# Kernel optimization log

Hardware: AMD Instinct MI355X
Metric: run time of the kernel (lower is better)

The kernel has to match this reference:

```python
import jax, jax.numpy as jnp
import numpy as np

BS, SEQ_LEN, DIM = 8, 16, 512
DIM_QK, DIM_V = 512, 512
MAX_BS, MAX_SEQ = 8, 8192
START_POS = 4096
KV_LEN = START_POS + SEQ_LEN


def setup_inputs() -> dict:
    key = jax.random.key(0)
    ks = jax.random.split(key, 8)
    w_scale = 0.02
    return {
        "x": jax.random.normal(ks[0], (BS, SEQ_LEN, DIM), dtype=jnp.float32),
        "start_pos": START_POS,
        "mask": jnp.zeros((SEQ_LEN, KV_LEN), dtype=jnp.float32),
        "Wq": jax.random.normal(ks[1], (DIM_QK, DIM), dtype=jnp.float32) * w_scale,
        "Wk": jax.random.normal(ks[2], (DIM_QK, DIM), dtype=jnp.float32) * w_scale,
        "Wv": jax.random.normal(ks[3], (DIM_V, DIM), dtype=jnp.float32) * w_scale,
        "Wo": jax.random.normal(ks[4], (DIM, DIM_V), dtype=jnp.float32) * w_scale,
        "cache_k": jax.random.normal(ks[5], (MAX_BS, MAX_SEQ, DIM_QK), dtype=jnp.float32) * 0.1,
        "cache_v": jax.random.normal(ks[6], (MAX_BS, MAX_SEQ, DIM_V), dtype=jnp.float32) * 0.1,
    }


def reference(x, start_pos, mask, Wq, Wk, Wv, Wo, cache_k, cache_v):
    bs, seq_len, _ = x.shape
    dim_qk = Wq.shape[0]
    scale = (dim_qk // 2) ** (-0.5)  # note: source uses dim_qk//2, not dim_qk

    # projections (torch Linear: y = x @ W.T, W is [out, in])
    q = jnp.einsum('bsd,ed->bse', x, Wq)
    k = jnp.einsum('bsd,ed->bse', x, Wk)
    v = jnp.einsum('bsd,ed->bse', x, Wv)

    # KV-cache append + read (start_pos is static)
    cache_k = jax.lax.dynamic_update_slice(cache_k, k, (0, start_pos, 0))
    cache_v = jax.lax.dynamic_update_slice(cache_v, v, (0, start_pos, 0))
    k_full = cache_k[:bs, :start_pos + seq_len]  # [bs, kv_len, dim_qk]
    v_full = cache_v[:bs, :start_pos + seq_len]  # [bs, kv_len, dim_v]

    dist = jnp.einsum('bqd,bkd->bqk', q, k_full) * scale  # [bs, q, kv]
    weight = jax.lax.stop_gradient(dist)
    dist = dist + mask  # additive mask, broadcast over batch
    probs = jax.nn.softmax(dist, axis=-1)
    atten = jnp.einsum('bqk,bkv->bqv', probs, v_full)
    out = jnp.einsum('bqv,ev->bqe', atten, Wo)
    return (out, weight)
```

## Files before the change

### kernel.cpp

```cpp
#include <hip/hip_runtime.h>

#define BSZ 8
#define SEQ 16
#define DIMN 512
#define SP 4096
#define KVL 4112

#define SCALE 0.0625f

#define QBUF  0
#define KNEW  65536
#define VNEW  131072
#define PROBS 196608
#define APART 722944
#define ATTEN 4982784

__device__ __forceinline__ float tree16(const float* acc, bool b1, bool b2, bool b4, bool b8)
{
  float r8[8];
#pragma unroll
  for (int u = 0; u < 8; ++u) {
    float keep = b1 ? acc[u + 8] : acc[u];
    float send = b1 ? acc[u] : acc[u + 8];
    r8[u] = keep + __shfl_xor(send, 1);
  }
  float r4[4];
#pragma unroll
  for (int u = 0; u < 4; ++u) {
    float keep = b2 ? r8[u + 4] : r8[u];
    float send = b2 ? r8[u] : r8[u + 4];
    r4[u] = keep + __shfl_xor(send, 2);
  }
  float r2[2];
#pragma unroll
  for (int u = 0; u < 2; ++u) {
    float keep = b4 ? r4[u + 2] : r4[u];
    float send = b4 ? r4[u] : r4[u + 2];
    r2[u] = keep + __shfl_xor(send, 4);
  }
  float keep = b8 ? r2[1] : r2[0];
  float send = b8 ? r2[0] : r2[1];
  float r1 = keep + __shfl_xor(send, 8);
  r1 += __shfl_xor(r1, 16);
  r1 += __shfl_xor(r1, 32);
  return r1;
}

__global__ __launch_bounds__(256) void proj_dot(
    const float* __restrict__ X,
    const float* __restrict__ W0, const float* __restrict__ W1,
    const float* __restrict__ W2,
    float* __restrict__ D0, float* __restrict__ D1, float* __restrict__ D2)
{
  int b = blockIdx.x;
  int e0 = blockIdx.y * 32;
  int t = threadIdx.x, lane = t & 63, w = t >> 6;

  float4 xa[SEQ], xb[SEQ];
  const float* xbase = X + (size_t)b * SEQ * DIMN + lane * 8;
#pragma unroll
  for (int s = 0; s < SEQ; ++s) {
    xa[s] = *(const float4*)(xbase + s * DIMN);
    xb[s] = *(const float4*)(xbase + s * DIMN + 4);
  }

  bool b1 = (lane & 1), b2 = (lane & 2), b4 = (lane & 4), b8 = (lane & 8);
#pragma unroll 2
  for (int i = 0; i < 8; ++i) {
    int e = e0 + w + 4 * i;
    int m = e >> 9, col = e & 511;
    const float* W = (m == 0) ? W0 : (m == 1) ? W1 : W2;
    const float* wrow = W + (size_t)col * DIMN + lane * 8;
    float4 ka = *(const float4*)(wrow);
    float4 kb = *(const float4*)(wrow + 4);

    float acc[SEQ];
#pragma unroll
    for (int s = 0; s < SEQ; ++s) {
      acc[s] = xa[s].x * ka.x + xa[s].y * ka.y + xa[s].z * ka.z + xa[s].w * ka.w
             + xb[s].x * kb.x + xb[s].y * kb.y + xb[s].z * kb.z + xb[s].w * kb.w;
    }
    float r1 = tree16(acc, b1, b2, b4, b8);
    if (lane < 16) {
      int s = ((lane & 1) << 3) | ((lane & 2) << 1) | ((lane & 4) >> 1) | ((lane & 8) >> 3);
      float* D = (m == 0) ? D0 : (m == 1) ? D1 : D2;
      D[(size_t)(b * SEQ + s) * DIMN + col] = r1;
    }
  }
}

__global__ __launch_bounds__(256) void scores_kernel(
    const float* __restrict__ qbuf, const float* __restrict__ cache_k,
    const float* __restrict__ knew, float* __restrict__ weight)
{
  int b = blockIdx.x;
  int p0 = blockIdx.y * 64;
  int len = KVL - p0; if (len > 64) len = 64;
  int t = threadIdx.x, lane = t & 63, w = t >> 6;

  float4 qa[SEQ], qb[SEQ];
  const float* qbase = qbuf + (size_t)b * SEQ * DIMN + lane * 8;
#pragma unroll
  for (int s = 0; s < SEQ; ++s) {
    qa[s] = *(const float4*)(qbase + s * DIMN);
    qb[s] = *(const float4*)(qbase + s * DIMN + 4);
  }

  bool b1 = (lane & 1), b2 = (lane & 2), b4 = (lane & 4), b8 = (lane & 8);
  int niter = (len - w + 3) >> 2;
#pragma unroll 2
  for (int i = 0; i < niter; ++i) {
    int p = p0 + w + 4 * i;
    const float* krow = (p < SP)
        ? (cache_k + ((size_t)b * 8192 + p) * DIMN)
        : (knew + (size_t)(b * SEQ + (p - SP)) * DIMN);
    float4 ka = *(const float4*)(krow + lane * 8);
    float4 kb = *(const float4*)(krow + lane * 8 + 4);

    float acc[SEQ];
#pragma unroll
    for (int s = 0; s < SEQ; ++s) {
      acc[s] = qa[s].x * ka.x + qa[s].y * ka.y + qa[s].z * ka.z + qa[s].w * ka.w
             + qb[s].x * kb.x + qb[s].y * kb.y + qb[s].z * kb.z + qb[s].w * kb.w;
    }
    float r1 = tree16(acc, b1, b2, b4, b8);
    if (lane < 16) {
      int s = ((lane & 1) << 3) | ((lane & 2) << 1) | ((lane & 4) >> 1) | ((lane & 8) >> 3);
      weight[(size_t)(b * SEQ + s) * KVL + p] = r1 * SCALE;
    }
  }
}

__global__ __launch_bounds__(256) void softmax_kernel(
    const float* __restrict__ weight, const float* __restrict__ mask,
    float* __restrict__ probs)
{
  int row = blockIdx.x;
  int s = row & 15;
  int t = threadIdx.x, lane = t & 63, w = t >> 6;
  const float* src = weight + (size_t)row * KVL;
  const float* msk = mask + (size_t)s * KVL;

  float vals[17];
  float mx = -1e30f;
#pragma unroll
  for (int i = 0; i < 17; ++i) {
    int p = t + i * 256;
    if (p < KVL) { vals[i] = src[p] + msk[p]; mx = fmaxf(mx, vals[i]); }
    else vals[i] = -1e30f;
  }
  for (int off = 32; off >= 1; off >>= 1) mx = fmaxf(mx, __shfl_xor(mx, off));
  __shared__ float redm[4], reds[4];
  if (lane == 0) redm[w] = mx;
  __syncthreads();
  mx = fmaxf(fmaxf(redm[0], redm[1]), fmaxf(redm[2], redm[3]));

  float sum = 0.f;
#pragma unroll
  for (int i = 0; i < 17; ++i) {
    int p = t + i * 256;
    if (p < KVL) { vals[i] = __expf(vals[i] - mx); sum += vals[i]; }
  }
  for (int off = 32; off >= 1; off >>= 1) sum += __shfl_xor(sum, off);
  if (lane == 0) reds[w] = sum;
  __syncthreads();
  sum = reds[0] + reds[1] + reds[2] + reds[3];
  float inv = 1.0f / sum;

  float* dst = probs + (size_t)row * KVL;
#pragma unroll
  for (int i = 0; i < 17; ++i) {
    int p = t + i * 256;
    if (p < KVL) dst[p] = vals[i] * inv;
  }
}

__global__ __launch_bounds__(256) void attnv_kernel(
    const float* __restrict__ probs, const float* __restrict__ cache_v,
    const float* __restrict__ vnew, float* __restrict__ apart)
{
  __shared__ float pl[SEQ][64];
  int b = blockIdx.x, c = blockIdx.y;
  int p0 = c * 64;
  int len = KVL - p0; if (len > 64) len = 64;
  int t = threadIdx.x;

  for (int i = t; i < SEQ * 64; i += 256) {
    int q = i >> 6, j = i & 63;
    pl[q][j] = (j < len) ? probs[(size_t)(b * SEQ + q) * KVL + p0 + j] : 0.f;
  }
  __syncthreads();

  float acc0[SEQ], acc1[SEQ];
#pragma unroll
  for (int q = 0; q < SEQ; ++q) { acc0[q] = 0.f; acc1[q] = 0.f; }

  int nj4 = len >> 2;
  for (int j4 = 0; j4 < nj4; ++j4) {
    float4 pv[SEQ];
#pragma unroll
    for (int q = 0; q < SEQ; ++q) pv[q] = *(const float4*)&pl[q][j4 * 4];
#pragma unroll
    for (int jj = 0; jj < 4; ++jj) {
      int p = p0 + j4 * 4 + jj;
      const float* vrow = (p < SP)
          ? (cache_v + ((size_t)b * 8192 + p) * DIMN)
          : (vnew + (size_t)(b * SEQ + (p - SP)) * DIMN);
      float va = vrow[t], vb = vrow[t + 256];
#pragma unroll
      for (int q = 0; q < SEQ; ++q) {
        float pj = (jj == 0) ? pv[q].x : (jj == 1) ? pv[q].y : (jj == 2) ? pv[q].z : pv[q].w;
        acc0[q] += pj * va;
        acc1[q] += pj * vb;
      }
    }
  }
  float* outp = apart + (size_t)c * 65536 + (size_t)b * SEQ * DIMN;
#pragma unroll
  for (int q = 0; q < SEQ; ++q) {
    outp[q * DIMN + t] = acc0[q];
    outp[q * DIMN + t + 256] = acc1[q];
  }
}

__global__ __launch_bounds__(256) void reduce_att(
    const float* __restrict__ apart, float* __restrict__ atten)
{
  int idx = blockIdx.x * 256 + threadIdx.x;
  float s = 0.f;
  for (int c = 0; c < 65; ++c) s += apart[(size_t)c * 65536 + idx];
  atten[idx] = s;
}

extern "C" void kernel_launch(void* const* d_in, const int* in_sizes, int n_in,
                              void* d_out, int out_size, void* d_ws, size_t ws_size,
                              hipStream_t stream) {
  const float* x       = (const float*)d_in[0];
  const float* mask    = (const float*)d_in[2];
  const float* Wq      = (const float*)d_in[3];
  const float* Wk      = (const float*)d_in[4];
  const float* Wv      = (const float*)d_in[5];
  const float* Wo      = (const float*)d_in[6];
  const float* cache_k = (const float*)d_in[7];
  const float* cache_v = (const float*)d_in[8];
  float* out    = (float*)d_out;
  float* weight = out + 65536;
  float* ws     = (float*)d_ws;

  proj_dot<<<dim3(8, 48), 256, 0, stream>>>(
      x, Wq, Wk, Wv, ws + QBUF, ws + KNEW, ws + VNEW);
  scores_kernel<<<dim3(8, 65), 256, 0, stream>>>(ws + QBUF, cache_k, ws + KNEW, weight);
  softmax_kernel<<<dim3(128), 256, 0, stream>>>(weight, mask, ws + PROBS);
  attnv_kernel<<<dim3(8, 65), 256, 0, stream>>>(ws + PROBS, cache_v, ws + VNEW, ws + APART);
  reduce_att<<<dim3(256), 256, 0, stream>>>(ws + APART, ws + ATTEN);
  proj_dot<<<dim3(8, 16), 256, 0, stream>>>(
      ws + ATTEN, Wo, Wo, Wo, out, out, out);
}
```

Baseline: 310.0 us.

## Fuse scores, softmax and attn-V into a flash-decoding split-KV kernel

Merges the score, softmax and probability-times-V kernels into one kernel per (batch, 64-key chunk). Each block keeps its scores in shared memory, computes a local max and sum, and writes unnormalized partial outputs. A new reduce kernel rescales and combines the partials across chunks using the saved max and sum values. This drops the round-trip of the probability matrix through global memory and two kernel launches, at the cost of extra exp work and a heavier final reduction.

```diff
diff --git a/kernel.cpp b/kernel.cpp
--- a/kernel.cpp
+++ b/kernel.cpp
@@ -11,9 +11,11 @@
 #define QBUF  0
 #define KNEW  65536
 #define VNEW  131072
-#define PROBS 196608
-#define APART 722944
-#define ATTEN 4982784
+#define MLBUF 196608
+#define APART 213248
+#define ATTEN 4473088
+
+#define MLSTRIDE 8320
 
 __device__ __forceinline__ float tree16(const float* acc, bool b1, bool b2, bool b4, bool b8)
 {
@@ -89,105 +91,79 @@
   }
 }
 
-__global__ __launch_bounds__(256) void scores_kernel(
+__global__ __launch_bounds__(256) void fused_attn(
     const float* __restrict__ qbuf, const float* __restrict__ cache_k,
-    const float* __restrict__ knew, float* __restrict__ weight)
-{
-  int b = blockIdx.x;
-  int p0 = blockIdx.y * 64;
-  int len = KVL - p0; if (len > 64) len = 64;
-  int t = threadIdx.x, lane = t & 63, w = t >> 6;
-
-  float4 qa[SEQ], qb[SEQ];
-  const float* qbase = qbuf + (size_t)b * SEQ * DIMN + lane * 8;
-#pragma unroll
-  for (int s = 0; s < SEQ; ++s) {
-    qa[s] = *(const float4*)(qbase + s * DIMN);
-    qb[s] = *(const float4*)(qbase + s * DIMN + 4);
-  }
-
-  bool b1 = (lane & 1), b2 = (lane & 2), b4 = (lane & 4), b8 = (lane & 8);
-  int niter = (len - w + 3) >> 2;
-#pragma unroll 2
-  for (int i = 0; i < niter; ++i) {
-    int p = p0 + w + 4 * i;
-    const float* krow = (p < SP)
-        ? (cache_k + ((size_t)b * 8192 + p) * DIMN)
-        : (knew + (size_t)(b * SEQ + (p - SP)) * DIMN);
-    float4 ka = *(const float4*)(krow + lane * 8);
-    float4 kb = *(const float4*)(krow + lane * 8 + 4);
-
-    float acc[SEQ];
-#pragma unroll
-    for (int s = 0; s < SEQ; ++s) {
-      acc[s] = qa[s].x * ka.x + qa[s].y * ka.y + qa[s].z * ka.z + qa[s].w * ka.w
-             + qb[s].x * kb.x + qb[s].y * kb.y + qb[s].z * kb.z + qb[s].w * kb.w;
-    }
-    float r1 = tree16(acc, b1, b2, b4, b8);
-    if (lane < 16) {
-      int s = ((lane & 1) << 3) | ((lane & 2) << 1) | ((lane & 4) >> 1) | ((lane & 8) >> 3);
-      weight[(size_t)(b * SEQ + s) * KVL + p] = r1 * SCALE;
-    }
-  }
-}
-
-__global__ __launch_bounds__(256) void softmax_kernel(
-    const float* __restrict__ weight, const float* __restrict__ mask,
-    float* __restrict__ probs)
-{
-  int row = blockIdx.x;
-  int s = row & 15;
-  int t = threadIdx.x, lane = t & 63, w = t >> 6;
-  const float* src = weight + (size_t)row * KVL;
-  const float* msk = mask + (size_t)s * KVL;
-
-  float vals[17];
-  float mx = -1e30f;
-#pragma unroll
-  for (int i = 0; i < 17; ++i) {
-    int p = t + i * 256;
-    if (p < KVL) { vals[i] = src[p] + msk[p]; mx = fmaxf(mx, vals[i]); }
-    else vals[i] = -1e30f;
-  }
-  for (int off = 32; off >= 1; off >>= 1) mx = fmaxf(mx, __shfl_xor(mx, off));
-  __shared__ float redm[4], reds[4];
-  if (lane == 0) redm[w] = mx;
-  __syncthreads();
-  mx = fmaxf(fmaxf(redm[0], redm[1]), fmaxf(redm[2], redm[3]));
-
-  float sum = 0.f;
-#pragma unroll
-  for (int i = 0; i < 17; ++i) {
-    int p = t + i * 256;
-    if (p < KVL) { vals[i] = __expf(vals[i] - mx); sum += vals[i]; }
-  }
-  for (int off = 32; off >= 1; off >>= 1) sum += __shfl_xor(sum, off);
-  if (lane == 0) reds[w] = sum;
-  __syncthreads();
-  sum = reds[0] + reds[1] + reds[2] + reds[3];
-  float inv = 1.0f / sum;
-
-  float* dst = probs + (size_t)row * KVL;
-#pragma unroll
-  for (int i = 0; i < 17; ++i) {
-    int p = t + i * 256;
-    if (p < KVL) dst[p] = vals[i] * inv;
-  }
-}
-
-__global__ __launch_bounds__(256) void attnv_kernel(
-    const float* __restrict__ probs, const float* __restrict__ cache_v,
-    const float* __restrict__ vnew, float* __restrict__ apart)
+    const float* __restrict__ knew, const float* __restrict__ mask,
+    const float* __restrict__ cache_v, const float* __restrict__ vnew,
+    float* __restrict__ weight, float* __restrict__ apart,
+    float* __restrict__ mlbuf)
 {
   __shared__ float pl[SEQ][64];
+  __shared__ float lm[SEQ], ll[SEQ];
   int b = blockIdx.x, c = blockIdx.y;
   int p0 = c * 64;
   int len = KVL - p0; if (len > 64) len = 64;
-  int t = threadIdx.x;
-
-  for (int i = t; i < SEQ * 64; i += 256) {
-    int q = i >> 6, j = i & 63;
-    pl[q][j] = (j < len) ? probs[(size_t)(b * SEQ + q) * KVL + p0 + j] : 0.f;
+  int t = threadIdx.x, lane = t & 63, w = t >> 6;
+
+  {
+    float4 qa[SEQ], qb[SEQ];
+    const float* qbase = qbuf + (size_t)b * SEQ * DIMN + lane * 8;
+#pragma unroll
+    for (int s = 0; s < SEQ; ++s) {
+      qa[s] = *(const float4*)(qbase + s * DIMN);
+      qb[s] = *(const float4*)(qbase + s * DIMN + 4);
+    }
+    bool b1 = (lane & 1), b2 = (lane & 2), b4 = (lane & 4), b8 = (lane & 8);
+    int niter = (len - w + 3) >> 2;
+#pragma unroll 2
+    for (int i = 0; i < niter; ++i) {
+      int p = p0 + w + 4 * i;
+      const float* krow = (p < SP)
+          ? (cache_k + ((size_t)b * 8192 + p) * DIMN)
+          : (knew + (size_t)(b * SEQ + (p - SP)) * DIMN);
+      float4 ka = *(const float4*)(krow + lane * 8);
+      float4 kb = *(const float4*)(krow + lane * 8 + 4);
+
+      float acc[SEQ];
+#pragma unroll
+      for (int s = 0; s < SEQ; ++s) {
+        acc[s] = qa[s].x * ka.x + qa[s].y * ka.y + qa[s].z * ka.z + qa[s].w * ka.w
+               + qb[s].x * kb.x + qb[s].y * kb.y + qb[s].z * kb.z + qb[s].w * kb.w;
+      }
+      float r1 = tree16(acc, b1, b2, b4, b8);
+      if (lane < 16) {
+        int s = ((lane & 1) << 3) | ((lane & 2) << 1) | ((lane & 4) >> 1) | ((lane & 8) >> 3);
+        float sc = r1 * SCALE;
+        weight[(size_t)(b * SEQ + s) * KVL + p] = sc;
+        pl[s][p - p0] = sc;
+      }
+    }
+  }
+  __syncthreads();
+
+  {
+    int r = t >> 4, j0 = (t & 15) * 4;
+    float v[4];
+#pragma unroll
+    for (int k = 0; k < 4; ++k) {
+      int j = j0 + k;
+      v[k] = (j < len) ? pl[r][j] + mask[r * KVL + p0 + j] : -1e30f;
+    }
+    float m = fmaxf(fmaxf(v[0], v[1]), fmaxf(v[2], v[3]));
+    m = fmaxf(m, __shfl_xor(m, 1));
+    m = fmaxf(m, __shfl_xor(m, 2));
+    m = fmaxf(m, __shfl_xor(m, 4));
+    m = fmaxf(m, __shfl_xor(m, 8));
+    float e[4], sum = 0.f;
+#pragma unroll
+    for (int k = 0; k < 4; ++k) { e[k] = __expf(v[k] - m); sum += e[k]; }
+    sum += __shfl_xor(sum, 1);
+    sum += __shfl_xor(sum, 2);
+    sum += __shfl_xor(sum, 4);
+    sum += __shfl_xor(sum, 8);
+#pragma unroll
+    for (int k = 0; k < 4; ++k) pl[r][j0 + k] = e[k];
+    if ((t & 15) == 0) { lm[r] = m; ll[r] = sum; }
   }
   __syncthreads();
 
@@ -221,15 +197,40 @@
     outp[q * DIMN + t] = acc0[q];
     outp[q * DIMN + t + 256] = acc1[q];
   }
-}
-
-__global__ __launch_bounds__(256) void reduce_att(
-    const float* __restrict__ apart, float* __restrict__ atten)
-{
-  int idx = blockIdx.x * 256 + threadIdx.x;
+  if (t < SEQ) {
+    mlbuf[c * 128 + b * SEQ + t] = lm[t];
+    mlbuf[MLSTRIDE + c * 128 + b * SEQ + t] = ll[t];
+  }
+}
+
+__global__ __launch_bounds__(256) void flash_reduce(
+    const float* __restrict__ apart, const float* __restrict__ mlbuf,
+    float* __restrict__ atten)
+{
+  __shared__ float msh[65], lsh[65], wfac[65];
+  int row = blockIdx.x >> 1, half = blockIdx.x & 1;
+  int t = threadIdx.x;
+
+  if (t < 65) {
+    msh[t] = mlbuf[t * 128 + row];
+    lsh[t] = mlbuf[MLSTRIDE + t * 128 + row];
+  }
+  __syncthreads();
+
+  float M = -1e30f;
+  for (int c = 0; c < 65; ++c) M = fmaxf(M, msh[c]);
+  if (t < 65) wfac[t] = __expf(msh[t] - M);
+  __syncthreads();
+
+  float L = 0.f;
+  for (int c = 0; c < 65; ++c) L += wfac[c] * lsh[c];
+  float inv = 1.0f / L;
+
+  int col = half * 256 + t;
+  const float* src = apart + (size_t)row * DIMN + col;
   float s = 0.f;
-  for (int c = 0; c < 65; ++c) s += apart[(size_t)c * 65536 + idx];
-  atten[idx] = s;
+  for (int c = 0; c < 65; ++c) s += wfac[c] * src[(size_t)c * 65536];
+  atten[(size_t)row * DIMN + col] = s * inv;
 }
 
 extern "C" void kernel_launch(void* const* d_in, const int* in_sizes, int n_in,
@@ -249,10 +250,11 @@
 
   proj_dot<<<dim3(8, 48), 256, 0, stream>>>(
       x, Wq, Wk, Wv, ws + QBUF, ws + KNEW, ws + VNEW);
-  scores_kernel<<<dim3(8, 65), 256, 0, stream>>>(ws + QBUF, cache_k, ws + KNEW, weight);
-  softmax_kernel<<<dim3(128), 256, 0, stream>>>(weight, mask, ws + PROBS);
-  attnv_kernel<<<dim3(8, 65), 256, 0, stream>>>(ws + PROBS, cache_v, ws + VNEW, ws + APART);
-  reduce_att<<<dim3(256), 256, 0, stream>>>(ws + APART, ws + ATTEN);
+  fused_attn<<<dim3(8, 65), 256, 0, stream>>>(
+      ws + QBUF, cache_k, ws + KNEW, mask, cache_v, ws + VNEW,
+      weight, ws + APART, ws + MLBUF);
+  flash_reduce<<<dim3(256), 256, 0, stream>>>(
+      ws + APART, ws + MLBUF, ws + ATTEN);
   proj_dot<<<dim3(8, 16), 256, 0, stream>>>(
       ws + ATTEN, Wo, Wo, Wo, out, out, out);
 }
```

Result: faster. 301.1 us (-2.9%).
